# Kernel tuning notes

Measured on AMD Instinct MI355X. Metric: run time of the kernel, lower is better.

## Reference

```python
import jax, jax.numpy as jnp
import numpy as np

W_CUB = 0.1
W_CD = 1.0
W_EXT = 0.01
W_SPS = 0.01
THRED = 24.0
COS_EPS = 1e-4

# cube face buffers (6 faces x 3 coords)
MASK_PROJECT = jnp.array([[0,1,1],[0,1,1],[1,0,1],[1,0,1],[1,1,0],[1,1,0]], jnp.float32)
MASK_PLANE   = jnp.array([[1,0,0],[1,0,0],[0,1,0],[0,1,0],[0,0,1],[0,0,1]], jnp.float32)
CUBE_NORMAL  = jnp.array([[-1,0,0],[1,0,0],[0,-1,0],[0,1,0],[0,0,-1],[0,0,1]], jnp.float32)
# torch repeat(...,3,...) of [[-1,-1,-1],[1,1,1]] tiles it -> [c0,c1,c0,c1,c0,c1]
CUBE_PLANES6 = jnp.tile(jnp.array([[-1.,-1.,-1.],[1.,1.,1.]], jnp.float32), (3,1))


def setup_inputs():
    B, P, N, S = 4, 24, 3072, 128
    key = jax.random.key(0)
    ks = jax.random.split(key, 8)
    pc_inver = jax.random.normal(ks[0], (B, P, N, 3), jnp.float32)
    normals_inver = jax.random.normal(ks[1], (B, P, N, 3), jnp.float32)
    scale = jax.random.uniform(ks[2], (B, P, 3), jnp.float32) * 0.9 + 0.1
    shape = jax.random.uniform(ks[3], (B, P, 2), jnp.float32) * 1.3 + 0.2
    exist = jax.random.uniform(ks[4], (B, P, 1), jnp.float32) * 0.98 + 0.01
    assign_matrix = jax.nn.softmax(jax.random.normal(ks[5], (B, N, P), jnp.float32), axis=-1)
    etas = jax.random.uniform(ks[6], (B, P, S), jnp.float32, minval=-jnp.pi/2, maxval=jnp.pi/2)
    omegas = jax.random.uniform(ks[7], (B, P, S), jnp.float32, minval=-jnp.pi, maxval=jnp.pi)
    return dict(pc_inver=pc_inver, normals_inver=normals_inver, scale=scale,
                shape=shape, exist=exist, assign_matrix=assign_matrix,
                etas=etas, omegas=omegas)


def _fexp(x, p):
    return jnp.sign(x) * jnp.abs(x) ** p


def _sample_sq_points(scale, eps, etas, omegas):
    # scale (B,P,3), eps (B,P,2), etas/omegas (B,P,S) -> (B,P,S,3)
    etas = jnp.where(etas == 0, 1e-6, etas)
    omegas = jnp.where(omegas == 0, 1e-6, omegas)
    a1, a2, a3 = scale[..., 0:1], scale[..., 1:2], scale[..., 2:3]
    e1, e2 = eps[..., 0:1], eps[..., 1:2]
    ce, se = jnp.cos(etas), jnp.sin(etas)
    co, so = jnp.cos(omegas), jnp.sin(omegas)
    x = a1 * _fexp(ce, e1) * _fexp(co, e2)
    y = a2 * _fexp(ce, e1) * _fexp(so, e2)
    z = a3 * _fexp(se, e1)
    fix = lambda v: (jnp.where(v > 0, 1.0, -1.0)) * jnp.maximum(jnp.abs(v), 1e-6)
    return jnp.stack([fix(x), fix(y), fix(z)], -1)


def _cd_loss(pc_inver, scale, shape, exist, assign_matrix, etas, omegas):
    X = _sample_sq_points(scale, shape, etas, omegas)          # (B,P,S,3)
    diff = X[:, :, :, None, :] - pc_inver[:, :, None, :, :]    # (B,P,S,N,3)
    D = jnp.sum(diff * diff, -1)                               # (B,P,S,N)
    pcl2prim = jnp.min(D, axis=2)                              # (B,P,N)
    pcl_loss = jnp.mean(jnp.sum(jnp.swapaxes(pcl2prim, 1, 2) * assign_matrix, -1))
    prim2pcl = jnp.mean(jnp.min(D, axis=3), axis=-1)           # (B,P)
    e = exist[..., 0]
    prim_loss = jnp.mean(jnp.sum(prim2pcl * e, -1) / (jnp.sum(e, -1) + 1e-6))
    return pcl_loss, prim_loss


def _cuboid_loss(pc_inver, normals_inver, scale, assign_matrix):
    pc = jnp.swapaxes(pc_inver, 1, 2)        # (B,N,P,3)
    nrm = jnp.swapaxes(normals_inver, 1, 2)  # (B,N,P,3)
    n_norm = jnp.maximum(jnp.linalg.norm(nrm, axis=-1, keepdims=True), COS_EPS)
    cos = jnp.einsum('bnpc,fc->bnpf', nrm, CUBE_NORMAL) / n_norm  # ||cube_normal||=1
    idx = jnp.argmax(cos, axis=-1)           # (B,N,P)
    s = scale[:, None, :, None, :]           # (B,1,P,1,3)
    proj = pc[:, :, :, None, :] * MASK_PROJECT + (CUBE_PLANES6 * s) * MASK_PLANE  # (B,N,P,6,3)
    proj = jnp.clip(proj, -s, s)
    proj_sel = jnp.take_along_axis(proj, idx[..., None, None], axis=3)[..., 0, :]  # (B,N,P,3)
    d = jnp.sum((proj_sel - pc) ** 2, -1)    # (B,N,P)
    return jnp.mean(jnp.sum(d * assign_matrix, -1))


def _common_losses(assign_matrix, exist):
    gt = jax.lax.stop_gradient((jnp.sum(assign_matrix, 1) > THRED).astype(jnp.float32))  # (B,P)
    p = exist[..., 0]
    bce = -jnp.mean(gt * jnp.log(p) + (1.0 - gt) * jnp.log1p(-p))
    N = assign_matrix.shape[1]
    sps = jnp.mean(jnp.mean(jnp.sqrt(jnp.sum(assign_matrix, 1) / N + 0.01), -1) ** 2)
    return bce, sps


def reference(pc_inver, normals_inver, scale, shape, exist, assign_matrix, etas, omegas):
    cub = _cuboid_loss(pc_inver, normals_inver, scale, assign_matrix)
    pcl_loss, prim_loss = _cd_loss(pc_inver, scale, shape, exist, assign_matrix, etas, omegas)
    bce, sps = _common_losses(assign_matrix, exist)
    return W_CUB * cub + W_CD * (pcl_loss + prim_loss) + W_EXT * bce + W_SPS * sps
```

## Files before the change

### kernel.cpp

```cpp
#include <hip/hip_runtime.h>
#include <math.h>

#define BB 4
#define PP 24
#define NN 3072
#define SS 128
#define CHUNK 512
#define NSPLIT 6
#define GRID (BB * PP * NSPLIT)
#define FINF 3.4e38f

#define SMIN_F  0
#define SCAL_F  (96 * SS * 8)
#define BPRES_F (SCAL_F + 96 * NSPLIT * 4)
#define CNT_F   (BPRES_F + 96 * 4)

__device__ __forceinline__ float fexp_f(float v, float p) {
    float m = powf(fabsf(v), p);
    float s = (v > 0.f) ? 1.f : ((v < 0.f) ? -1.f : 0.f);
    return s * m;
}
__device__ __forceinline__ float fix_f(float v) {
    return ((v > 0.f) ? 1.f : -1.f) * fmaxf(fabsf(v), 1e-6f);
}
__device__ __forceinline__ float wave_sum(float v) {
    #pragma unroll
    for (int off = 32; off > 0; off >>= 1) v += __shfl_down(v, off);
    return v;
}
__device__ __forceinline__ float aload(const float* p) {
    return __hip_atomic_load(p, __ATOMIC_RELAXED, __HIP_MEMORY_SCOPE_AGENT);
}
__device__ __forceinline__ void astore(float* p, float v) {
    __hip_atomic_store(p, v, __ATOMIC_RELAXED, __HIP_MEMORY_SCOPE_AGENT);
}
__device__ __forceinline__ float cub_dist(float px, float py, float pz,
                                          float nx, float ny, float nz,
                                          float sc0, float sc1, float sc2) {
    float best = -nx; int idx = 0;
    if ( nx > best) { best =  nx; idx = 1; }
    if (-ny > best) { best = -ny; idx = 2; }
    if ( ny > best) { best =  ny; idx = 3; }
    if (-nz > best) { best = -nz; idx = 4; }
    if ( nz > best) { best =  nz; idx = 5; }
    const int c = idx >> 1;
    const float scc = (c == 0) ? sc0 : ((c == 1) ? sc1 : sc2);
    const float fv  = (idx & 1) ? scc : -scc;
    float pr0 = (c == 0) ? fv : fminf(fmaxf(px, -sc0), sc0);
    float pr1 = (c == 1) ? fv : fminf(fmaxf(py, -sc1), sc1);
    float pr2 = (c == 2) ? fv : fminf(fmaxf(pz, -sc2), sc2);
    float d0 = pr0 - px, d1 = pr1 - py, d2 = pr2 - pz;
    return fmaf(d0, d0, fmaf(d1, d1, d2 * d2));
}

__global__ __launch_bounds__(128) void superdec_init(float* __restrict__ ws) {
    const int i = threadIdx.x;
    if (i < 97) ((unsigned*)(ws + CNT_F))[i] = 0u;
}

__global__ __launch_bounds__(256) void superdec_fused(
    const float* __restrict__ pc, const float* __restrict__ nrm,
    const float* __restrict__ scale, const float* __restrict__ shape,
    const float* __restrict__ exist, const float* __restrict__ assign,
    const float* __restrict__ etas, const float* __restrict__ omegas,
    float* __restrict__ ws, float* __restrict__ out)
{
    const int blk   = blockIdx.x;
    const int bp    = blk / NSPLIT;
    const int split = blk % NSPLIT;
    const int b     = bp / PP;
    const int p     = bp % PP;
    const int tid   = threadIdx.x;
    const int n0    = split * CHUNK;
    const int pg    = tid & 63;
    const int sg    = tid >> 6;

    __shared__ float4 Xs[SS];
    __shared__ float  s_red[4][32][68];
    __shared__ float4 dminL[4][64][2];
    __shared__ float4 cubam[128][2];
    __shared__ float  red[1024];
    __shared__ float  wsum[6];
    __shared__ unsigned s_cnt1, s_cnt2;

    const float sc0 = scale[bp * 3 + 0];
    const float sc1 = scale[bp * 3 + 1];
    const float sc2 = scale[bp * 3 + 2];

    const float4* pc4 = (const float4*)(pc + ((size_t)bp * NN + n0) * 3);
    float px[8], py[8], pz[8], psq[8];
    {
        const float4 g0 = pc4[pg * 6 + 0];
        const float4 g1 = pc4[pg * 6 + 1];
        const float4 g2 = pc4[pg * 6 + 2];
        const float4 g3 = pc4[pg * 6 + 3];
        const float4 g4 = pc4[pg * 6 + 4];
        const float4 g5 = pc4[pg * 6 + 5];
        px[0]=g0.x; py[0]=g0.y; pz[0]=g0.z;
        px[1]=g0.w; py[1]=g1.x; pz[1]=g1.y;
        px[2]=g1.z; py[2]=g1.w; pz[2]=g2.x;
        px[3]=g2.y; py[3]=g2.z; pz[3]=g2.w;
        px[4]=g3.x; py[4]=g3.y; pz[4]=g3.z;
        px[5]=g3.w; py[5]=g4.x; pz[5]=g4.y;
        px[6]=g4.z; py[6]=g4.w; pz[6]=g5.x;
        px[7]=g5.y; py[7]=g5.z; pz[7]=g5.w;
        #pragma unroll
        for (int j = 0; j < 8; ++j)
            psq[j] = fmaf(px[j], px[j], fmaf(py[j], py[j], pz[j] * pz[j]));
    }

    const int pid = tid & 127;
    const float4 a0 = pc4[pid * 3 + 0];
    const float4 a1 = pc4[pid * 3 + 1];
    const float4 a2 = pc4[pid * 3 + 2];
    const float qx0 = a0.x, qy0 = a0.y, qz0 = a0.z;
    const float qx1 = a0.w, qy1 = a1.x, qz1 = a1.y;
    const float qx2 = a1.z, qy2 = a1.w, qz2 = a2.x;
    const float qx3 = a2.y, qy3 = a2.z, qz3 = a2.w;
    const float qs0 = fmaf(qx0, qx0, fmaf(qy0, qy0, qz0 * qz0));
    const float qs1 = fmaf(qx1, qx1, fmaf(qy1, qy1, qz1 * qz1));
    const float qs2 = fmaf(qx2, qx2, fmaf(qy2, qy2, qz2 * qz2));
    const float qs3 = fmaf(qx3, qx3, fmaf(qy3, qy3, qz3 * qz3));

    if (tid < 128) {
        const float e1 = shape[bp * 2 + 0];
        const float e2 = shape[bp * 2 + 1];
        float eta = etas[bp * SS + tid];
        float omg = omegas[bp * SS + tid];
        eta = (eta == 0.f) ? 1e-6f : eta;
        omg = (omg == 0.f) ? 1e-6f : omg;
        float ce = cosf(eta), se = sinf(eta);
        float co = cosf(omg), so = sinf(omg);
        float fce = fexp_f(ce, e1);
        float x = fix_f(sc0 * fce * fexp_f(co, e2));
        float y = fix_f(sc1 * fce * fexp_f(so, e2));
        float z = fix_f(sc2 * fexp_f(se, e1));
        float xsq = fmaf(x, x, fmaf(y, y, z * z));
        Xs[tid] = make_float4(-2.f * x, -2.f * y, -2.f * z, xsq);
    } else {
        const float4* nr4 = (const float4*)(nrm + ((size_t)bp * NN + n0) * 3);
        const float4 h0 = nr4[pid * 3 + 0];
        const float4 h1 = nr4[pid * 3 + 1];
        const float4 h2 = nr4[pid * 3 + 2];
        float c0 = cub_dist(qx0, qy0, qz0, h0.x, h0.y, h0.z, sc0, sc1, sc2);
        float c1 = cub_dist(qx1, qy1, qz1, h0.w, h1.x, h1.y, sc0, sc1, sc2);
        float c2 = cub_dist(qx2, qy2, qz2, h1.z, h1.w, h2.x, sc0, sc1, sc2);
        float c3 = cub_dist(qx3, qy3, qz3, h2.y, h2.z, h2.w, sc0, sc1, sc2);
        const size_t abase = ((size_t)b * NN + n0 + pid * 4) * PP + p;
        const float m0 = assign[abase + 0 * PP];
        const float m1 = assign[abase + 1 * PP];
        const float m2 = assign[abase + 2 * PP];
        const float m3 = assign[abase + 3 * PP];
        cubam[pid][0] = make_float4(c0, c1, c2, c3);
        cubam[pid][1] = make_float4(m0, m1, m2, m3);
    }
    __syncthreads();

    {
        float pmin[8];
        #pragma unroll
        for (int j = 0; j < 8; ++j) pmin[j] = FINF;
        const int sb = sg * 32;
        #pragma unroll 4
        for (int k = 0; k < 32; ++k) {
            const float4 x = Xs[sb + k];
            float d0 = fmaf(x.x, px[0], fmaf(x.y, py[0], fmaf(x.z, pz[0], x.w)));
            float d1 = fmaf(x.x, px[1], fmaf(x.y, py[1], fmaf(x.z, pz[1], x.w)));
            float d2 = fmaf(x.x, px[2], fmaf(x.y, py[2], fmaf(x.z, pz[2], x.w)));
            float d3 = fmaf(x.x, px[3], fmaf(x.y, py[3], fmaf(x.z, pz[3], x.w)));
            float d4 = fmaf(x.x, px[4], fmaf(x.y, py[4], fmaf(x.z, pz[4], x.w)));
            float d5 = fmaf(x.x, px[5], fmaf(x.y, py[5], fmaf(x.z, pz[5], x.w)));
            float d6 = fmaf(x.x, px[6], fmaf(x.y, py[6], fmaf(x.z, pz[6], x.w)));
            float d7 = fmaf(x.x, px[7], fmaf(x.y, py[7], fmaf(x.z, pz[7], x.w)));
            pmin[0] = fminf(pmin[0], d0);
            pmin[1] = fminf(pmin[1], d1);
            pmin[2] = fminf(pmin[2], d2);
            pmin[3] = fminf(pmin[3], d3);
            pmin[4] = fminf(pmin[4], d4);
            pmin[5] = fminf(pmin[5], d5);
            pmin[6] = fminf(pmin[6], d6);
            pmin[7] = fminf(pmin[7], d7);
            const float e0 = d0 + psq[0], e1 = d1 + psq[1];
            const float e2 = d2 + psq[2], e3 = d3 + psq[3];
            const float e4 = d4 + psq[4], e5 = d5 + psq[5];
            const float e6 = d6 + psq[6], e7 = d7 + psq[7];
            const float sv = fminf(fminf(fminf(e0, e1), fminf(e2, e3)),
                                   fminf(fminf(e4, e5), fminf(e6, e7)));
            s_red[sg][k][pg] = sv;
        }
        dminL[sg][pg][0] = make_float4(pmin[0], pmin[1], pmin[2], pmin[3]);
        dminL[sg][pg][1] = make_float4(pmin[4], pmin[5], pmin[6], pmin[7]);
    }
    __syncthreads();

    if (tid < SS) {
        const int zg = tid >> 5, k = tid & 31;
        const float4* r4 = (const float4*)&s_red[zg][k][0];
        float m = FINF;
        #pragma unroll
        for (int i = 0; i < 16; ++i) {
            const float4 v = r4[i];
            m = fminf(fminf(fminf(m, v.x), v.y), fminf(v.z, v.w));
        }
        astore(ws + SMIN_F + ((bp * SS + tid) << 3) + split, m);

        const int pg2 = tid >> 1, hf = tid & 1;
        const float4 e0 = dminL[0][pg2][hf];
        const float4 e1 = dminL[1][pg2][hf];
        const float4 e2 = dminL[2][pg2][hf];
        const float4 e3 = dminL[3][pg2][hf];
        const float dd0 = fminf(fminf(e0.x, e1.x), fminf(e2.x, e3.x)) + qs0;
        const float dd1 = fminf(fminf(e0.y, e1.y), fminf(e2.y, e3.y)) + qs1;
        const float dd2 = fminf(fminf(e0.z, e1.z), fminf(e2.z, e3.z)) + qs2;
        const float dd3 = fminf(fminf(e0.w, e1.w), fminf(e2.w, e3.w)) + qs3;
        const float4 cb = cubam[tid][0];
        const float4 am = cubam[tid][1];
        const float acc_pcl = dd0 * am.x + dd1 * am.y + dd2 * am.z + dd3 * am.w;
        const float acc_cub = cb.x * am.x + cb.y * am.y + cb.z * am.z + cb.w * am.w;
        const float acc_am  = am.x + am.y + am.z + am.w;
        const float s0 = wave_sum(acc_pcl);
        const float s1 = wave_sum(acc_cub);
        const float s2 = wave_sum(acc_am);
        const int lane_ = tid & 63, wv = tid >> 6;
        if (lane_ == 0) {
            wsum[wv * 3 + 0] = s0;
            wsum[wv * 3 + 1] = s1;
            wsum[wv * 3 + 2] = s2;
        }
    }

    __syncthreads();
    if (tid == 0) {
        float* sc = ws + SCAL_F + (bp * NSPLIT + split) * 4;
        astore(sc + 0, wsum[0] + wsum[3]);
        astore(sc + 1, wsum[1] + wsum[4]);
        astore(sc + 2, wsum[2] + wsum[5]);
        asm volatile("s_waitcnt vmcnt(0)" ::: "memory");
        s_cnt1 = __hip_atomic_fetch_add((unsigned*)(ws + CNT_F) + bp, 1u,
                                        __ATOMIC_RELAXED, __HIP_MEMORY_SCOPE_AGENT);
    }
    __syncthreads();
    if (s_cnt1 != (unsigned)(NSPLIT - 1)) return;

    {
        const int lane = tid & 63;
        if (tid < SS) {
            const float* mb = ws + SMIN_F + ((bp * SS + tid) << 3);
            const float v0 = aload(mb + 0), v1 = aload(mb + 1), v2 = aload(mb + 2);
            const float v3 = aload(mb + 3), v4 = aload(mb + 4), v5 = aload(mb + 5);
            float m = fminf(fminf(fminf(v0, v1), fminf(v2, v3)), fminf(v4, v5));
            float sm = wave_sum(m);
            if (lane == 0) wsum[tid >> 6] = sm;
        } else if (tid < 128 + 18) {
            const int j = tid - 128, sp = j / 3, c = j % 3;
            red[600 + j] = aload(ws + SCAL_F + (bp * NSPLIT + sp) * 4 + c);
        }
        __syncthreads();
        if (tid == 0) {
            const float prim = wsum[0] + wsum[1];
            float pcl = 0.f, cubv = 0.f, cs = 0.f;
            #pragma unroll
            for (int sp = 0; sp < NSPLIT; ++sp) {
                pcl  += red[600 + sp * 3 + 0];
                cubv += red[600 + sp * 3 + 1];
                cs   += red[600 + sp * 3 + 2];
            }
            float* r4 = ws + BPRES_F + bp * 4;
            astore(r4 + 0, prim);
            astore(r4 + 1, pcl);
            astore(r4 + 2, cubv);
            astore(r4 + 3, cs);
            asm volatile("s_waitcnt vmcnt(0)" ::: "memory");
            s_cnt2 = __hip_atomic_fetch_add((unsigned*)(ws + CNT_F) + 96, 1u,
                                            __ATOMIC_RELAXED, __HIP_MEMORY_SCOPE_AGENT);
        }
        __syncthreads();
        if (s_cnt2 != 95u) return;
    }

    if (tid < 96) {
        const float* r4 = ws + BPRES_F + tid * 4;
        const float prim = aload(r4 + 0);
        const float pcl  = aload(r4 + 1);
        const float cubv = aload(r4 + 2);
        const float cs   = aload(r4 + 3);
        const float e  = exist[tid];
        const float gt = (cs > 24.0f) ? 1.f : 0.f;
        red[  0 + tid] = prim;
        red[ 96 + tid] = pcl;
        red[192 + tid] = cubv;
        red[288 + tid] = gt * logf(e) + (1.f - gt) * log1pf(-e);
        red[384 + tid] = e;
        red[480 + tid] = sqrtf(cs / (float)NN + 0.01f);
    }
    __syncthreads();

    if (tid == 0) {
        float pcl_sum = 0.f, cub_sum = 0.f, bce_sum = 0.f, prim_loss = 0.f, sps = 0.f;
        #pragma unroll
        for (int b_ = 0; b_ < BB; ++b_) {
            float pe = 0.f, ee = 0.f, sq = 0.f;
            #pragma unroll
            for (int p_ = 0; p_ < PP; ++p_) {
                const int i = b_ * PP + p_;
                pcl_sum += red[ 96 + i];
                cub_sum += red[192 + i];
                bce_sum += red[288 + i];
                pe += (red[i] / (float)SS) * red[384 + i];
                ee += red[384 + i];
                sq += red[480 + i];
            }
            prim_loss += pe / (ee + 1e-6f);
            float mb = sq / (float)PP;
            sps += mb * mb;
        }
        prim_loss /= (float)BB;
        sps       /= (float)BB;
        float pcl_loss = pcl_sum / (float)(BB * NN);
        float cubf     = cub_sum / (float)(BB * NN);
        float bce      = -bce_sum / (float)(BB * PP);
        out[0] = 0.1f * cubf + 1.0f * (pcl_loss + prim_loss) + 0.01f * bce + 0.01f * sps;
    }
}

extern "C" void kernel_launch(void* const* d_in, const int* in_sizes, int n_in,
                              void* d_out, int out_size, void* d_ws, size_t ws_size,
                              hipStream_t stream) {
    const float* pc     = (const float*)d_in[0];
    const float* nrm    = (const float*)d_in[1];
    const float* scale  = (const float*)d_in[2];
    const float* shape  = (const float*)d_in[3];
    const float* exist  = (const float*)d_in[4];
    const float* assign = (const float*)d_in[5];
    const float* etas   = (const float*)d_in[6];
    const float* omegas = (const float*)d_in[7];
    float* ws  = (float*)d_ws;
    float* out = (float*)d_out;

    superdec_init<<<1, 128, 0, stream>>>(ws);

    superdec_fused<<<GRID, 256, 0, stream>>>(
        pc, nrm, scale, shape, exist, assign, etas, omegas, ws, out);
}
```

Measured before the change: 89.61 us.

## Use one 1024-thread block per (batch,primitive) instead of split blocks

Replaces the 576-block grid (6 splits of 512 points per primitive, 256 threads) with 96 blocks of 1024 threads, each covering all 3072 points of one primitive. This removes the cross-block partial-minimum workspace and the first atomic counter stage. Each thread now handles 3 points and shuffles within groups of 8 lanes before writing to shared memory. The cost is much lower grid parallelism: 96 blocks on a GPU with far more CUs, plus a larger 128x132 shared reduction array and a longer loop over all 128 samples per thread.

```diff
diff --git a/kernel.cpp b/kernel.cpp
--- a/kernel.cpp
+++ b/kernel.cpp
@@ -5,15 +5,11 @@
 #define PP 24
 #define NN 3072
 #define SS 128
-#define CHUNK 512
-#define NSPLIT 6
-#define GRID (BB * PP * NSPLIT)
+#define GRID 96
 #define FINF 3.4e38f
 
-#define SMIN_F  0
-#define SCAL_F  (96 * SS * 8)
-#define BPRES_F (SCAL_F + 96 * NSPLIT * 4)
-#define CNT_F   (BPRES_F + 96 * 4)
+#define BPRES_F 0
+#define CNT_F   (96 * 4)
 
 __device__ __forceinline__ float fexp_f(float v, float p) {
     float m = powf(fabsf(v), p);
@@ -53,74 +49,41 @@
     return fmaf(d0, d0, fmaf(d1, d1, d2 * d2));
 }
 
-__global__ __launch_bounds__(128) void superdec_init(float* __restrict__ ws) {
-    const int i = threadIdx.x;
-    if (i < 97) ((unsigned*)(ws + CNT_F))[i] = 0u;
-}
-
-__global__ __launch_bounds__(256) void superdec_fused(
+__global__ __launch_bounds__(64) void superdec_init(float* __restrict__ ws) {
+    if (threadIdx.x == 0) *(unsigned*)(ws + CNT_F) = 0u;
+}
+
+__global__ __launch_bounds__(1024) void superdec_fused(
     const float* __restrict__ pc, const float* __restrict__ nrm,
     const float* __restrict__ scale, const float* __restrict__ shape,
     const float* __restrict__ exist, const float* __restrict__ assign,
     const float* __restrict__ etas, const float* __restrict__ omegas,
     float* __restrict__ ws, float* __restrict__ out)
 {
-    const int blk   = blockIdx.x;
-    const int bp    = blk / NSPLIT;
-    const int split = blk % NSPLIT;
-    const int b     = bp / PP;
-    const int p     = bp % PP;
-    const int tid   = threadIdx.x;
-    const int n0    = split * CHUNK;
-    const int pg    = tid & 63;
-    const int sg    = tid >> 6;
+    const int bp   = blockIdx.x;
+    const int b    = bp / PP;
+    const int p    = bp % PP;
+    const int tid  = threadIdx.x;
+    const int lane = tid & 63;
+    const int wv   = tid >> 6;
 
     __shared__ float4 Xs[SS];
-    __shared__ float  s_red[4][32][68];
-    __shared__ float4 dminL[4][64][2];
-    __shared__ float4 cubam[128][2];
-    __shared__ float  red[1024];
-    __shared__ float  wsum[6];
-    __shared__ unsigned s_cnt1, s_cnt2;
+    __shared__ float  s_red[SS][132];
+    __shared__ float  wsum[2];
+    __shared__ float  swv[16][4];
+    __shared__ unsigned s_cnt;
 
     const float sc0 = scale[bp * 3 + 0];
     const float sc1 = scale[bp * 3 + 1];
     const float sc2 = scale[bp * 3 + 2];
 
-    const float4* pc4 = (const float4*)(pc + ((size_t)bp * NN + n0) * 3);
-    float px[8], py[8], pz[8], psq[8];
-    {
-        const float4 g0 = pc4[pg * 6 + 0];
-        const float4 g1 = pc4[pg * 6 + 1];
-        const float4 g2 = pc4[pg * 6 + 2];
-        const float4 g3 = pc4[pg * 6 + 3];
-        const float4 g4 = pc4[pg * 6 + 4];
-        const float4 g5 = pc4[pg * 6 + 5];
-        px[0]=g0.x; py[0]=g0.y; pz[0]=g0.z;
-        px[1]=g0.w; py[1]=g1.x; pz[1]=g1.y;
-        px[2]=g1.z; py[2]=g1.w; pz[2]=g2.x;
-        px[3]=g2.y; py[3]=g2.z; pz[3]=g2.w;
-        px[4]=g3.x; py[4]=g3.y; pz[4]=g3.z;
-        px[5]=g3.w; py[5]=g4.x; pz[5]=g4.y;
-        px[6]=g4.z; py[6]=g4.w; pz[6]=g5.x;
-        px[7]=g5.y; py[7]=g5.z; pz[7]=g5.w;
-        #pragma unroll
-        for (int j = 0; j < 8; ++j)
-            psq[j] = fmaf(px[j], px[j], fmaf(py[j], py[j], pz[j] * pz[j]));
-    }
-
-    const int pid = tid & 127;
-    const float4 a0 = pc4[pid * 3 + 0];
-    const float4 a1 = pc4[pid * 3 + 1];
-    const float4 a2 = pc4[pid * 3 + 2];
-    const float qx0 = a0.x, qy0 = a0.y, qz0 = a0.z;
-    const float qx1 = a0.w, qy1 = a1.x, qz1 = a1.y;
-    const float qx2 = a1.z, qy2 = a1.w, qz2 = a2.x;
-    const float qx3 = a2.y, qy3 = a2.z, qz3 = a2.w;
-    const float qs0 = fmaf(qx0, qx0, fmaf(qy0, qy0, qz0 * qz0));
-    const float qs1 = fmaf(qx1, qx1, fmaf(qy1, qy1, qz1 * qz1));
-    const float qs2 = fmaf(qx2, qx2, fmaf(qy2, qy2, qz2 * qz2));
-    const float qs3 = fmaf(qx3, qx3, fmaf(qy3, qy3, qz3 * qz3));
+    const float3* pc3 = (const float3*)pc + (size_t)bp * NN;
+    const float3 P0 = pc3[tid];
+    const float3 P1 = pc3[tid + 1024];
+    const float3 P2 = pc3[tid + 2048];
+    const float psq0 = fmaf(P0.x, P0.x, fmaf(P0.y, P0.y, P0.z * P0.z));
+    const float psq1 = fmaf(P1.x, P1.x, fmaf(P1.y, P1.y, P1.z * P1.z));
+    const float psq2 = fmaf(P2.x, P2.x, fmaf(P2.y, P2.y, P2.z * P2.z));
 
     if (tid < 128) {
         const float e1 = shape[bp * 2 + 0];
@@ -137,147 +100,91 @@
         float z = fix_f(sc2 * fexp_f(se, e1));
         float xsq = fmaf(x, x, fmaf(y, y, z * z));
         Xs[tid] = make_float4(-2.f * x, -2.f * y, -2.f * z, xsq);
-    } else {
-        const float4* nr4 = (const float4*)(nrm + ((size_t)bp * NN + n0) * 3);
-        const float4 h0 = nr4[pid * 3 + 0];
-        const float4 h1 = nr4[pid * 3 + 1];
-        const float4 h2 = nr4[pid * 3 + 2];
-        float c0 = cub_dist(qx0, qy0, qz0, h0.x, h0.y, h0.z, sc0, sc1, sc2);
-        float c1 = cub_dist(qx1, qy1, qz1, h0.w, h1.x, h1.y, sc0, sc1, sc2);
-        float c2 = cub_dist(qx2, qy2, qz2, h1.z, h1.w, h2.x, sc0, sc1, sc2);
-        float c3 = cub_dist(qx3, qy3, qz3, h2.y, h2.z, h2.w, sc0, sc1, sc2);
-        const size_t abase = ((size_t)b * NN + n0 + pid * 4) * PP + p;
-        const float m0 = assign[abase + 0 * PP];
-        const float m1 = assign[abase + 1 * PP];
-        const float m2 = assign[abase + 2 * PP];
-        const float m3 = assign[abase + 3 * PP];
-        cubam[pid][0] = make_float4(c0, c1, c2, c3);
-        cubam[pid][1] = make_float4(m0, m1, m2, m3);
-    }
-    __syncthreads();
-
-    {
-        float pmin[8];
-        #pragma unroll
-        for (int j = 0; j < 8; ++j) pmin[j] = FINF;
-        const int sb = sg * 32;
-        #pragma unroll 4
-        for (int k = 0; k < 32; ++k) {
-            const float4 x = Xs[sb + k];
-            float d0 = fmaf(x.x, px[0], fmaf(x.y, py[0], fmaf(x.z, pz[0], x.w)));
-            float d1 = fmaf(x.x, px[1], fmaf(x.y, py[1], fmaf(x.z, pz[1], x.w)));
-            float d2 = fmaf(x.x, px[2], fmaf(x.y, py[2], fmaf(x.z, pz[2], x.w)));
-            float d3 = fmaf(x.x, px[3], fmaf(x.y, py[3], fmaf(x.z, pz[3], x.w)));
-            float d4 = fmaf(x.x, px[4], fmaf(x.y, py[4], fmaf(x.z, pz[4], x.w)));
-            float d5 = fmaf(x.x, px[5], fmaf(x.y, py[5], fmaf(x.z, pz[5], x.w)));
-            float d6 = fmaf(x.x, px[6], fmaf(x.y, py[6], fmaf(x.z, pz[6], x.w)));
-            float d7 = fmaf(x.x, px[7], fmaf(x.y, py[7], fmaf(x.z, pz[7], x.w)));
-            pmin[0] = fminf(pmin[0], d0);
-            pmin[1] = fminf(pmin[1], d1);
-            pmin[2] = fminf(pmin[2], d2);
-            pmin[3] = fminf(pmin[3], d3);
-            pmin[4] = fminf(pmin[4], d4);
-            pmin[5] = fminf(pmin[5], d5);
-            pmin[6] = fminf(pmin[6], d6);
-            pmin[7] = fminf(pmin[7], d7);
-            const float e0 = d0 + psq[0], e1 = d1 + psq[1];
-            const float e2 = d2 + psq[2], e3 = d3 + psq[3];
-            const float e4 = d4 + psq[4], e5 = d5 + psq[5];
-            const float e6 = d6 + psq[6], e7 = d7 + psq[7];
-            const float sv = fminf(fminf(fminf(e0, e1), fminf(e2, e3)),
-                                   fminf(fminf(e4, e5), fminf(e6, e7)));
-            s_red[sg][k][pg] = sv;
-        }
-        dminL[sg][pg][0] = make_float4(pmin[0], pmin[1], pmin[2], pmin[3]);
-        dminL[sg][pg][1] = make_float4(pmin[4], pmin[5], pmin[6], pmin[7]);
-    }
-    __syncthreads();
-
-    if (tid < SS) {
-        const int zg = tid >> 5, k = tid & 31;
-        const float4* r4 = (const float4*)&s_red[zg][k][0];
+    }
+
+    const float3* nr3 = (const float3*)nrm + (size_t)bp * NN;
+    const float3 N0 = nr3[tid];
+    const float3 N1 = nr3[tid + 1024];
+    const float3 N2 = nr3[tid + 2048];
+    const float cub0 = cub_dist(P0.x, P0.y, P0.z, N0.x, N0.y, N0.z, sc0, sc1, sc2);
+    const float cub1 = cub_dist(P1.x, P1.y, P1.z, N1.x, N1.y, N1.z, sc0, sc1, sc2);
+    const float cub2 = cub_dist(P2.x, P2.y, P2.z, N2.x, N2.y, N2.z, sc0, sc1, sc2);
+    const size_t abase = ((size_t)b * NN + tid) * PP + p;
+    const float am0 = assign[abase];
+    const float am1 = assign[abase + (size_t)1024 * PP];
+    const float am2 = assign[abase + (size_t)2048 * PP];
+    __syncthreads();
+
+    float pmin0 = FINF, pmin1 = FINF, pmin2 = FINF;
+    #pragma unroll 4
+    for (int k = 0; k < SS; ++k) {
+        const float4 x = Xs[k];
+        const float d0 = fmaf(x.x, P0.x, fmaf(x.y, P0.y, fmaf(x.z, P0.z, x.w)));
+        const float d1 = fmaf(x.x, P1.x, fmaf(x.y, P1.y, fmaf(x.z, P1.z, x.w)));
+        const float d2 = fmaf(x.x, P2.x, fmaf(x.y, P2.y, fmaf(x.z, P2.z, x.w)));
+        pmin0 = fminf(pmin0, d0);
+        pmin1 = fminf(pmin1, d1);
+        pmin2 = fminf(pmin2, d2);
+        float sv = fminf(fminf(d0 + psq0, d1 + psq1), d2 + psq2);
+        sv = fminf(sv, __shfl_xor(sv, 1));
+        sv = fminf(sv, __shfl_xor(sv, 2));
+        sv = fminf(sv, __shfl_xor(sv, 4));
+        if ((lane & 7) == 0) s_red[k][(wv << 3) | (lane >> 3)] = sv;
+    }
+    __syncthreads();
+
+    if (tid < 128) {
+        const float4* r4 = (const float4*)&s_red[tid][0];
         float m = FINF;
         #pragma unroll
-        for (int i = 0; i < 16; ++i) {
+        for (int i = 0; i < 32; ++i) {
             const float4 v = r4[i];
             m = fminf(fminf(fminf(m, v.x), v.y), fminf(v.z, v.w));
         }
-        astore(ws + SMIN_F + ((bp * SS + tid) << 3) + split, m);
-
-        const int pg2 = tid >> 1, hf = tid & 1;
-        const float4 e0 = dminL[0][pg2][hf];
-        const float4 e1 = dminL[1][pg2][hf];
-        const float4 e2 = dminL[2][pg2][hf];
-        const float4 e3 = dminL[3][pg2][hf];
-        const float dd0 = fminf(fminf(e0.x, e1.x), fminf(e2.x, e3.x)) + qs0;
-        const float dd1 = fminf(fminf(e0.y, e1.y), fminf(e2.y, e3.y)) + qs1;
-        const float dd2 = fminf(fminf(e0.z, e1.z), fminf(e2.z, e3.z)) + qs2;
-        const float dd3 = fminf(fminf(e0.w, e1.w), fminf(e2.w, e3.w)) + qs3;
-        const float4 cb = cubam[tid][0];
-        const float4 am = cubam[tid][1];
-        const float acc_pcl = dd0 * am.x + dd1 * am.y + dd2 * am.z + dd3 * am.w;
-        const float acc_cub = cb.x * am.x + cb.y * am.y + cb.z * am.z + cb.w * am.w;
-        const float acc_am  = am.x + am.y + am.z + am.w;
+        const float sm = wave_sum(m);
+        if (lane == 0) wsum[tid >> 6] = sm;
+    }
+
+    {
+        const float dd0 = pmin0 + psq0;
+        const float dd1 = pmin1 + psq1;
+        const float dd2 = pmin2 + psq2;
+        const float acc_pcl = dd0 * am0 + dd1 * am1 + dd2 * am2;
+        const float acc_cub = cub0 * am0 + cub1 * am1 + cub2 * am2;
+        const float acc_am  = am0 + am1 + am2;
         const float s0 = wave_sum(acc_pcl);
         const float s1 = wave_sum(acc_cub);
         const float s2 = wave_sum(acc_am);
-        const int lane_ = tid & 63, wv = tid >> 6;
-        if (lane_ == 0) {
-            wsum[wv * 3 + 0] = s0;
-            wsum[wv * 3 + 1] = s1;
-            wsum[wv * 3 + 2] = s2;
-        }
-    }
-
-    __syncthreads();
+        if (lane == 0) {
+            swv[wv][0] = s0;
+            swv[wv][1] = s1;
+            swv[wv][2] = s2;
+        }
+    }
+    __syncthreads();
+
     if (tid == 0) {
-        float* sc = ws + SCAL_F + (bp * NSPLIT + split) * 4;
-        astore(sc + 0, wsum[0] + wsum[3]);
-        astore(sc + 1, wsum[1] + wsum[4]);
-        astore(sc + 2, wsum[2] + wsum[5]);
+        const float prim = wsum[0] + wsum[1];
+        float pcl = 0.f, cubv = 0.f, cs = 0.f;
+        #pragma unroll
+        for (int w = 0; w < 16; ++w) {
+            pcl  += swv[w][0];
+            cubv += swv[w][1];
+            cs   += swv[w][2];
+        }
+        float* r4 = ws + BPRES_F + bp * 4;
+        astore(r4 + 0, prim);
+        astore(r4 + 1, pcl);
+        astore(r4 + 2, cubv);
+        astore(r4 + 3, cs);
         asm volatile("s_waitcnt vmcnt(0)" ::: "memory");
-        s_cnt1 = __hip_atomic_fetch_add((unsigned*)(ws + CNT_F) + bp, 1u,
-                                        __ATOMIC_RELAXED, __HIP_MEMORY_SCOPE_AGENT);
-    }
-    __syncthreads();
-    if (s_cnt1 != (unsigned)(NSPLIT - 1)) return;
-
-    {
-        const int lane = tid & 63;
-        if (tid < SS) {
-            const float* mb = ws + SMIN_F + ((bp * SS + tid) << 3);
-            const float v0 = aload(mb + 0), v1 = aload(mb + 1), v2 = aload(mb + 2);
-            const float v3 = aload(mb + 3), v4 = aload(mb + 4), v5 = aload(mb + 5);
-            float m = fminf(fminf(fminf(v0, v1), fminf(v2, v3)), fminf(v4, v5));
-            float sm = wave_sum(m);
-            if (lane == 0) wsum[tid >> 6] = sm;
-        } else if (tid < 128 + 18) {
-            const int j = tid - 128, sp = j / 3, c = j % 3;
-            red[600 + j] = aload(ws + SCAL_F + (bp * NSPLIT + sp) * 4 + c);
-        }
-        __syncthreads();
-        if (tid == 0) {
-            const float prim = wsum[0] + wsum[1];
-            float pcl = 0.f, cubv = 0.f, cs = 0.f;
-            #pragma unroll
-            for (int sp = 0; sp < NSPLIT; ++sp) {
-                pcl  += red[600 + sp * 3 + 0];
-                cubv += red[600 + sp * 3 + 1];
-                cs   += red[600 + sp * 3 + 2];
-            }
-            float* r4 = ws + BPRES_F + bp * 4;
-            astore(r4 + 0, prim);
-            astore(r4 + 1, pcl);
-            astore(r4 + 2, cubv);
-            astore(r4 + 3, cs);
-            asm volatile("s_waitcnt vmcnt(0)" ::: "memory");
-            s_cnt2 = __hip_atomic_fetch_add((unsigned*)(ws + CNT_F) + 96, 1u,
-                                            __ATOMIC_RELAXED, __HIP_MEMORY_SCOPE_AGENT);
-        }
-        __syncthreads();
-        if (s_cnt2 != 95u) return;
-    }
-
+        s_cnt = __hip_atomic_fetch_add((unsigned*)(ws + CNT_F), 1u,
+                                       __ATOMIC_RELAXED, __HIP_MEMORY_SCOPE_AGENT);
+    }
+    __syncthreads();
+    if (s_cnt != (unsigned)(GRID - 1)) return;
+
+    float* red = &s_red[0][0];
     if (tid < 96) {
         const float* r4 = ws + BPRES_F + tid * 4;
         const float prim = aload(r4 + 0);
@@ -337,8 +244,8 @@
     float* ws  = (float*)d_ws;
     float* out = (float*)d_out;
 
-    superdec_init<<<1, 128, 0, stream>>>(ws);
-
-    superdec_fused<<<GRID, 256, 0, stream>>>(
+    superdec_init<<<1, 64, 0, stream>>>(ws);
+
+    superdec_fused<<<GRID, 1024, 0, stream>>>(
         pc, nrm, scale, shape, exist, assign, etas, omegas, ws, out);
 }
```

Result: slower. 107.1 us (+19.5%).
